# Optimization experiments

Hardware: AMD Instinct MI355X
Metric: run time of the kernel (lower is better)

The kernel has to match this reference:

```python
import jax, jax.numpy as jnp
import numpy as np

def binarize(t):
    # deterministic sign binarization to {-1, +1}
    return jnp.where(t >= 0, 1.0, -1.0).astype(t.dtype)

def setup_inputs() -> dict:
    key = jax.random.key(0)
    k1, k2 = jax.random.split(key)
    x = jax.random.normal(k1, (8192, 4096), dtype=jnp.float32)
    kernel = jax.random.normal(k2, (4096, 4096), dtype=jnp.float32)
    return {"x": x, "kernel": kernel}

def reference(x, kernel):
    # BinaryLayer.call with binary=True: matmul(binarize(x), binarize(W))
    return jnp.matmul(binarize(x), binarize(kernel))
```

## Files before the change

### kernel.cpp

```cpp
#include <hip/hip_runtime.h>
#include <stdint.h>

#define MDIM 8192
#define NDIM 4096
#define KDIM 4096
#define KB2  (KDIM / 2)
#define BKB  128
#define NKT  (KDIM / 256)

typedef __attribute__((ext_vector_type(4))) int   i32x4;
typedef __attribute__((ext_vector_type(8))) int   i32x8;
typedef __attribute__((ext_vector_type(4))) float f32x4;

__device__ __forceinline__ void gload16(const void* g, void* l) {
    __builtin_amdgcn_global_load_lds(
        (const __attribute__((address_space(1))) void*)g,
        (__attribute__((address_space(3))) void*)l, 16, 0, 0);
}

__device__ __forceinline__ i32x8 pad8(i32x4 v) {
    i32x8 r;
    r[0] = v[0]; r[1] = v[1]; r[2] = v[2]; r[3] = v[3];
    r[4] = 0;    r[5] = 0;    r[6] = 0;    r[7] = 0;
    return r;
}

#define MFMA_FP4(a, b, c)                                                   \
    __builtin_amdgcn_mfma_scale_f32_16x16x128_f8f6f4(                        \
        (a), (b), (c), 4, 4, 0, 0x7F7F7F7F, 0, 0x7F7F7F7F)

__global__ __launch_bounds__(256) void pack_a4_kernel(const float* __restrict__ X,
                                                      uint8_t* __restrict__ A4) {
    size_t gt = (size_t)blockIdx.x * 256 + threadIdx.x;
    const float4* x4 = (const float4*)X + gt * 4;
    uint32_t out[2] = {0, 0};
#pragma unroll
    for (int q = 0; q < 4; ++q) {
        float4 v = x4[q];
        uint32_t b0 = (v.x >= 0.f ? 0x2u : 0xAu) | ((v.y >= 0.f ? 0x2u : 0xAu) << 4);
        uint32_t b1 = (v.z >= 0.f ? 0x2u : 0xAu) | ((v.w >= 0.f ? 0x2u : 0xAu) << 4);
        out[q >> 1] |= (b0 | (b1 << 8)) << ((q & 1) * 16);
    }
    ((uint2*)A4)[gt] = make_uint2(out[0], out[1]);
}

__global__ __launch_bounds__(256) void pack_b4t_kernel(const float* __restrict__ W,
                                                       uint8_t* __restrict__ B4) {
    __shared__ uint8_t t[64][72];
    const int tid = threadIdx.x;
    const int k0 = blockIdx.y * 64, n0 = blockIdx.x * 64;
#pragma unroll
    for (int r = 0; r < 4; ++r) {
        int e  = r * 1024 + tid * 4;
        int k  = e >> 6;
        int nn = e & 63;
        float4 v = *(const float4*)&W[(size_t)(k0 + k) * NDIM + n0 + nn];
        uint32_t b0 = (v.x >= 0.f) ? 0x2u : 0xAu;
        uint32_t b1 = (v.y >= 0.f) ? 0x2u : 0xAu;
        uint32_t b2 = (v.z >= 0.f) ? 0x2u : 0xAu;
        uint32_t b3 = (v.w >= 0.f) ? 0x2u : 0xAu;
        *(uint32_t*)&t[k][nn] = b0 | (b1 << 8) | (b2 << 16) | (b3 << 24);
    }
    __syncthreads();
    const int n = tid >> 2, kc = tid & 3;
    uint32_t w[2] = {0, 0};
#pragma unroll
    for (int b = 0; b < 8; ++b) {
        int k = kc * 16 + b * 2;
        uint32_t byte = (uint32_t)t[k][n] | ((uint32_t)t[k + 1][n] << 4);
        w[b >> 2] |= byte << ((b & 3) * 8);
    }
    *(uint2*)&B4[(size_t)(n0 + n) * KB2 + k0 / 2 + kc * 8] = make_uint2(w[0], w[1]);
}

__global__ __launch_bounds__(256) void binmm_fp4_kernel(const uint8_t* __restrict__ A4,
                                                        const uint8_t* __restrict__ B4,
                                                        float* __restrict__ C) {
    __shared__ uint8_t As[128 * 128];
    __shared__ uint8_t Bs[128 * 128];

    const int tid = threadIdx.x, lane = tid & 63, wid = tid >> 6;
    const int wr = wid >> 1, wc = wid & 1;
    const int l15 = lane & 15, g = lane >> 4;
    const int m0 = blockIdx.y * 128, n0 = blockIdx.x * 128;

    const int srow  = tid >> 3;
    const int sslot = tid & 7;
    const uint8_t* gA[4];
    const uint8_t* gB[4];
    uint8_t* dA[4];
    uint8_t* dB[4];
#pragma unroll
    for (int p = 0; p < 4; ++p) {
        int row = srow + p * 32;
        int ss  = (sslot ^ (row & 7)) * 16;
        gA[p] = A4 + (size_t)(m0 + row) * KB2 + ss;
        gB[p] = B4 + (size_t)(n0 + row) * KB2 + ss;
        dA[p] = As + p * 4096 + tid * 16;
        dB[p] = Bs + p * 4096 + tid * 16;
    }

    f32x4 acc[4][4];
#pragma unroll
    for (int m = 0; m < 4; ++m)
#pragma unroll
        for (int n = 0; n < 4; ++n) acc[m][n] = (f32x4){0.f, 0.f, 0.f, 0.f};

    for (int kt = 0; kt < NKT; ++kt) {
#pragma unroll
        for (int p = 0; p < 4; ++p) {
            gload16(gA[p], dA[p]);
            gload16(gB[p], dB[p]);
            gA[p] += BKB;
            gB[p] += BKB;
        }
        __syncthreads();
#pragma unroll
        for (int s = 0; s < 2; ++s) {
            i32x8 af[4], bf[4];
#pragma unroll
            for (int m = 0; m < 4; ++m) {
                int row  = wr * 64 + m * 16 + l15;
                int slot = ((s * 4 + g) ^ (row & 7)) * 16;
                af[m] = pad8(*(const i32x4*)(As + row * 128 + slot));
            }
#pragma unroll
            for (int n = 0; n < 4; ++n) {
                int row  = wc * 64 + n * 16 + l15;
                int slot = ((s * 4 + g) ^ (row & 7)) * 16;
                bf[n] = pad8(*(const i32x4*)(Bs + row * 128 + slot));
            }
#pragma unroll
            for (int m = 0; m < 4; ++m)
#pragma unroll
                for (int n = 0; n < 4; ++n)
                    acc[m][n] = MFMA_FP4(af[m], bf[n], acc[m][n]);
        }
        __syncthreads();
    }

#pragma unroll
    for (int m = 0; m < 4; ++m) {
#pragma unroll
        for (int n = 0; n < 4; ++n) {
            size_t cc = (size_t)(n0 + wc * 64 + n * 16 + l15);
            int rbase = m0 + wr * 64 + m * 16 + g * 4;
#pragma unroll
            for (int reg = 0; reg < 4; ++reg)
                C[(size_t)(rbase + reg) * NDIM + cc] = acc[m][n][reg];
        }
    }
}

extern "C" void kernel_launch(void* const* d_in, const int* in_sizes, int n_in,
                              void* d_out, int out_size, void* d_ws, size_t ws_size,
                              hipStream_t stream) {
    const float* x = (const float*)d_in[0];
    const float* w = (const float*)d_in[1];
    float* out = (float*)d_out;

    uint8_t* A4 = (uint8_t*)d_ws;
    uint8_t* B4 = (uint8_t*)d_ws + (size_t)MDIM * KB2;

    pack_a4_kernel<<<(int)((size_t)MDIM * KDIM / 16 / 256), 256, 0, stream>>>(x, A4);
    pack_b4t_kernel<<<dim3(NDIM / 64, KDIM / 64), 256, 0, stream>>>(w, B4);
    binmm_fp4_kernel<<<dim3(NDIM / 128, MDIM / 128), 256, 0, stream>>>(A4, B4, out);
}
```

Measured before the change: 132.3 us.

## Enlarge GEMM tile to 256x256 with 512 threads and double-buffered LDS prefetch

The FP4 MFMA GEMM moves from 128x128 tiles with 4 waves to 256x256 tiles with 8 waves, each wave computing a 128x64 sub-tile. LDS is double-buffered so the next K-slice's global-to-LDS loads are issued before the current slice's MFMAs, and one barrier per iteration is removed. MFMA sections are wrapped in s_setprio to favour issuing math. The aim is more reuse per loaded byte and overlap of memory with compute. The cost is 128 KB of LDS per block and higher register pressure, and the launch bounds of 2 blocks per CU may not be achievable with that LDS use.

```diff
diff --git a/kernel.cpp b/kernel.cpp
--- a/kernel.cpp
+++ b/kernel.cpp
@@ -7,6 +7,11 @@
 #define KB2  (KDIM / 2)
 #define BKB  128
 #define NKT  (KDIM / 256)
+
+#define BM 256
+#define BN 256
+#define ABUF      32768
+#define BUFSTRIDE 65536
 
 typedef __attribute__((ext_vector_type(4))) int   i32x4;
 typedef __attribute__((ext_vector_type(8))) int   i32x8;
@@ -73,78 +78,91 @@
     *(uint2*)&B4[(size_t)(n0 + n) * KB2 + k0 / 2 + kc * 8] = make_uint2(w[0], w[1]);
 }
 
-__global__ __launch_bounds__(256) void binmm_fp4_kernel(const uint8_t* __restrict__ A4,
-                                                        const uint8_t* __restrict__ B4,
-                                                        float* __restrict__ C) {
-    __shared__ uint8_t As[128 * 128];
-    __shared__ uint8_t Bs[128 * 128];
+__global__ __launch_bounds__(512, 2) void binmm_fp4_kernel(const uint8_t* __restrict__ A4,
+                                                           const uint8_t* __restrict__ B4,
+                                                           float* __restrict__ C) {
+    __shared__ uint8_t lds[2 * BUFSTRIDE];
 
     const int tid = threadIdx.x, lane = tid & 63, wid = tid >> 6;
-    const int wr = wid >> 1, wc = wid & 1;
-    const int l15 = lane & 15, g = lane >> 4;
-    const int m0 = blockIdx.y * 128, n0 = blockIdx.x * 128;
+    const int wr = wid >> 2, wc = wid & 3;
+    const int l15 = lane & 15, g = (lane >> 4) & 3;
+    const int m0 = blockIdx.y * BM, n0 = blockIdx.x * BN;
 
     const int srow  = tid >> 3;
     const int sslot = tid & 7;
     const uint8_t* gA[4];
     const uint8_t* gB[4];
-    uint8_t* dA[4];
-    uint8_t* dB[4];
 #pragma unroll
     for (int p = 0; p < 4; ++p) {
-        int row = srow + p * 32;
+        int row = srow + p * 64;
         int ss  = (sslot ^ (row & 7)) * 16;
         gA[p] = A4 + (size_t)(m0 + row) * KB2 + ss;
         gB[p] = B4 + (size_t)(n0 + row) * KB2 + ss;
-        dA[p] = As + p * 4096 + tid * 16;
-        dB[p] = Bs + p * 4096 + tid * 16;
     }
 
-    f32x4 acc[4][4];
+    f32x4 acc[8][4];
 #pragma unroll
-    for (int m = 0; m < 4; ++m)
+    for (int m = 0; m < 8; ++m)
 #pragma unroll
         for (int n = 0; n < 4; ++n) acc[m][n] = (f32x4){0.f, 0.f, 0.f, 0.f};
 
-    for (int kt = 0; kt < NKT; ++kt) {
 #pragma unroll
-        for (int p = 0; p < 4; ++p) {
-            gload16(gA[p], dA[p]);
-            gload16(gB[p], dB[p]);
-            gA[p] += BKB;
-            gB[p] += BKB;
+    for (int p = 0; p < 4; ++p) {
+        gload16(gA[p], lds + tid * 16 + p * 8192);
+        gload16(gB[p], lds + ABUF + tid * 16 + p * 8192);
+        gA[p] += BKB;
+        gB[p] += BKB;
+    }
+    __syncthreads();
+
+    int cur = 0;
+    for (int t = 0; t < NKT; ++t) {
+        if (t + 1 < NKT) {
+            uint8_t* nb = lds + (cur ^ 1) * BUFSTRIDE;
+#pragma unroll
+            for (int p = 0; p < 4; ++p) {
+                gload16(gA[p], nb + tid * 16 + p * 8192);
+                gload16(gB[p], nb + ABUF + tid * 16 + p * 8192);
+                gA[p] += BKB;
+                gB[p] += BKB;
+            }
         }
-        __syncthreads();
+
+        const uint8_t* Acur = lds + cur * BUFSTRIDE;
+        const uint8_t* Bcur = Acur + ABUF;
 #pragma unroll
         for (int s = 0; s < 2; ++s) {
-            i32x8 af[4], bf[4];
-#pragma unroll
-            for (int m = 0; m < 4; ++m) {
-                int row  = wr * 64 + m * 16 + l15;
-                int slot = ((s * 4 + g) ^ (row & 7)) * 16;
-                af[m] = pad8(*(const i32x4*)(As + row * 128 + slot));
-            }
+            i32x8 bf[4];
 #pragma unroll
             for (int n = 0; n < 4; ++n) {
                 int row  = wc * 64 + n * 16 + l15;
                 int slot = ((s * 4 + g) ^ (row & 7)) * 16;
-                bf[n] = pad8(*(const i32x4*)(Bs + row * 128 + slot));
+                bf[n] = pad8(*(const i32x4*)(Bcur + row * 128 + slot));
             }
+            __builtin_amdgcn_s_setprio(1);
 #pragma unroll
-            for (int m = 0; m < 4; ++m)
-#pragma unroll
-                for (int n = 0; n < 4; ++n)
-                    acc[m][n] = MFMA_FP4(af[m], bf[n], acc[m][n]);
+            for (int m = 0; m < 8; ++m) {
+                int row  = wr * 128 + m * 16 + l15;
+                int slot = ((s * 4 + g) ^ (row & 7)) * 16;
+                i32x8 af = pad8(*(const i32x4*)(Acur + row * 128 + slot));
+                acc[m][0] = MFMA_FP4(af, bf[0], acc[m][0]);
+                acc[m][1] = MFMA_FP4(af, bf[1], acc[m][1]);
+                acc[m][2] = MFMA_FP4(af, bf[2], acc[m][2]);
+                acc[m][3] = MFMA_FP4(af, bf[3], acc[m][3]);
+            }
+            __builtin_amdgcn_s_setprio(0);
         }
+
         __syncthreads();
+        cur ^= 1;
     }
 
 #pragma unroll
-    for (int m = 0; m < 4; ++m) {
+    for (int m = 0; m < 8; ++m) {
 #pragma unroll
         for (int n = 0; n < 4; ++n) {
             size_t cc = (size_t)(n0 + wc * 64 + n * 16 + l15);
-            int rbase = m0 + wr * 64 + m * 16 + g * 4;
+            int rbase = m0 + wr * 128 + m * 16 + g * 4;
 #pragma unroll
             for (int reg = 0; reg < 4; ++reg)
                 C[(size_t)(rbase + reg) * NDIM + cc] = acc[m][n][reg];
@@ -164,5 +182,5 @@
 
     pack_a4_kernel<<<(int)((size_t)MDIM * KDIM / 16 / 256), 256, 0, stream>>>(x, A4);
     pack_b4t_kernel<<<dim3(NDIM / 64, KDIM / 64), 256, 0, stream>>>(w, B4);
-    binmm_fp4_kernel<<<dim3(NDIM / 128, MDIM / 128), 256, 0, stream>>>(A4, B4, out);
+    binmm_fp4_kernel<<<dim3(NDIM / BN, MDIM / BM), 512, 0, stream>>>(A4, B4, out);
 }
```

Measured after the change: 124.8 us. -5.7%, faster.
